# Performance work log

Measured on AMD Instinct MI355X. Metric: run time of the kernel, lower is better.

Reference implementation:

```python
import jax, jax.numpy as jnp
import numpy as np

B, F, K = 8192, 128, 32  # batch, num_features, bins per feature (D = F*K = 4096)
T_TOTAL = 1000           # num_timesteps for the cosine schedule
EPS_LOG = 1e-8
EPS_GUMBEL = 1e-30


def _cosine_sigmas(T):
    # matches _make_schedule('cosine', T)
    steps = jnp.arange(T + 1, dtype=jnp.float32)
    alphas_cumprod = jnp.cos((steps / T + 0.008) / 1.008 * jnp.pi / 2) ** 2
    return 1.0 - alphas_cumprod[1:] / alphas_cumprod[:-1]  # [T]


def setup_inputs() -> dict:
    key = jax.random.key(0)
    k1, k2 = jax.random.split(key)
    # log one-hot x0, as built in mixed_loss: log(one_hot + 1e-8)
    x0 = jax.random.randint(k1, (B, F), 0, K)
    log_x0 = jnp.log(jax.nn.one_hot(x0, K, dtype=jnp.float32) + EPS_LOG).reshape(B, F * K)
    # uniform noise for the Gumbel-max trick (rand_like in the original)
    u = jax.random.uniform(k2, (B, F * K), dtype=jnp.float32)
    return {"log_x0": log_x0, "u": u, "t": 64}


def reference(log_x0, u, t):
    # q_sample: t sequential q_forward steps, fused over features via a scan.
    sigmas = _cosine_sigmas(T_TOTAL)[:t]          # [t], t is a static Python int
    Q = jnp.ones((K, K), jnp.float32) / K         # fixed uniform score matrix

    def step(log_p, sigma_t):
        p = jnp.exp(log_p)                                     # [B,F,K]
        p_next = (1.0 - sigma_t) * p + sigma_t * jnp.einsum('bfi,ij->bfj', p, Q)
        return jnp.log(p_next + EPS_LOG), None

    log_p0 = log_x0.reshape(B, F, K)
    log_p, _ = jax.lax.scan(step, log_p0, sigmas)              # [B,F,K]

    # log_sample_categorical: Gumbel-max per feature block
    g = -jnp.log(-jnp.log(u.reshape(B, F, K) + EPS_GUMBEL) + EPS_GUMBEL)
    sample = jnp.argmax(log_p + g, axis=-1)                    # [B,F]
    log_xt = jnp.log(jax.nn.one_hot(sample, K, dtype=jnp.float32) + EPS_LOG)
    return log_xt.reshape(B, F * K)
```

## Files before the change

kernel.cpp:

```cpp
#include <hip/hip_runtime.h>
#include <math.h>


typedef float f4nt __attribute__((ext_vector_type(4)));

__device__ __forceinline__ float cr_logf32(float x) { return (float)log((double)x); }

__device__ __forceinline__ float cr_g(float u) {
    float c0 = __fadd_rn(u, 1e-30f);
    float t2 = cr_logf32(c0);
    float t3 = __fadd_rn(-t2, 1e-30f);
    float t4 = cr_logf32(t3);
    return -t4;
}

__global__ void traj_kernel(const float* __restrict__ log_x0,
                            const int* __restrict__ t_ptr,
                            float* __restrict__ traj) {
    __shared__ float ac[1001];
    __shared__ float sig[1000];
    __shared__ float init2[2];
    int t = *t_ptr;
    if (t > 1000) t = 1000;
    if (t < 0) t = 0;

    for (int s = threadIdx.x; s <= t; s += blockDim.x) {
        float a = __fdiv_rn((float)s, 1000.0f);
        float b = __fadd_rn(a, 0.008f);
        float c = __fdiv_rn(b, 1.008f);
        float d = __fmul_rn(c, 0x1.921fb6p+1f);
        float e = __fmul_rn(d, 0.5f);
        float cs = (float)cos((double)e);
        ac[s] = __fmul_rn(cs, cs);
    }
    if (threadIdx.x == 0) {
        float hotf = -1e30f, coldf = 1e30f;
        for (int j = 0; j < 32; ++j) {
            float v = log_x0[j];
            hotf = fmaxf(hotf, v);
            coldf = fminf(coldf, v);
        }
        init2[0] = hotf;
        init2[1] = coldf;
        traj[64] = coldf;
    }
    __syncthreads();
    for (int s = threadIdx.x + 1; s <= t; s += blockDim.x)
        sig[s - 1] = __fsub_rn(1.0f, __fdiv_rn(ac[s], ac[s - 1]));
    __syncthreads();

    if (threadIdx.x < 32) {
        const int h = threadIdx.x;
        float lh = init2[0];
        float lc = init2[1];
        for (int k = 0; k < t; ++k) {
            float sg = sig[k];
            float ph = (float)exp((double)lh);
            float pc = (float)exp((double)lc);
            float th = __fmul_rn(ph, 0.03125f);
            float tc = __fmul_rn(pc, 0.03125f);
            float acc = 0.0f;
            for (int i = 0; i < 32; ++i)
                acc = __fadd_rn(acc, (i == h) ? th : tc);
            float s1  = __fsub_rn(1.0f, sg);
            float sm  = __fmul_rn(sg, acc);
            float phn = __fadd_rn(__fmul_rn(s1, ph), sm);
            float pcn = __fadd_rn(__fmul_rn(s1, pc), sm);
            lh = cr_logf32(__fadd_rn(phn, 1e-8f));
            lc = cr_logf32(__fadd_rn(pcn, 1e-8f));
        }
        traj[h]      = lh;
        traj[32 + h] = lc;
    }
}

#define SCANB(VAL, IDX)                                         \
    {                                                           \
        const float cu = ((IDX) == hc) ? -1.0f : (VAL);         \
        const bool gt1 = cu > t1u;                              \
        const bool gt2 = cu > t2u;                              \
        t2u = gt1 ? t1u : (gt2 ? cu : t2u);                     \
        t1i = gt1 ? (IDX) : t1i;                                \
        t1u = gt1 ? cu : t1u;                                   \
    }

__global__ void sample_kernel(const float4* __restrict__ log_x0,
                              const float4* __restrict__ u,
                              const float* __restrict__ trajm,
                              float4* __restrict__ out) {
    __shared__ float lds_u[4][2048];
    __shared__ unsigned char lds_h[4][64];
    __shared__ float lh_s[32], lc_s[32];
    __shared__ float coldv_s;
    if (threadIdx.x < 32) {
        lh_s[threadIdx.x] = trajm[threadIdx.x];
        lc_s[threadIdx.x] = trajm[32 + threadIdx.x];
    }
    if (threadIdx.x == 0) coldv_s = trajm[64];

    const int w    = threadIdx.x >> 6;
    const int lane = threadIdx.x & 63;
    const int tile = (int)((blockIdx.x * blockDim.x + threadIdx.x) >> 6);
    const size_t fb4 = (size_t)tile * 512;

    float4 xr[8];
    #pragma unroll
    for (int k = 0; k < 8; ++k) xr[k] = log_x0[fb4 + k * 64 + lane];
    float4 ur[8];
    #pragma unroll
    for (int k = 0; k < 8; ++k) ur[k] = u[fb4 + k * 64 + lane];

    const int sgb = lane & ~7;
    #pragma unroll
    for (int k = 0; k < 8; ++k) {
        const float4 xv = xr[k];
        int p = -1;
        p = (xv.x > -1.0f) ? 0 : p;
        p = (xv.y > -1.0f) ? 1 : p;
        p = (xv.z > -1.0f) ? 2 : p;
        p = (xv.w > -1.0f) ? 3 : p;
        const unsigned long long bal = __ballot(p >= 0);
        const unsigned mm = (unsigned)((bal >> sgb) & 0xFFull);
        const int hlane = (int)__ffs(mm) - 1;
        const int psrc  = __shfl(p, sgb + ((hlane < 0) ? 0 : hlane), 64);
        const int hbin  = (hlane < 0) ? 255 : (hlane * 4 + psrc);
        if ((lane & 7) == 0)
            lds_h[w][k * 8 + (lane >> 3)] = (unsigned char)hbin;
    }

    #pragma unroll
    for (int k = 0; k < 8; ++k)
        *(float4*)&lds_u[w][k * 256 + lane * 4] = ur[k];

    __syncthreads();

    const int   h  = (int)lds_h[w][lane];
    const int   hc = (h > 31) ? 0 : h;
    const float lh = lh_s[hc];
    const float lc = lc_s[hc];
    const float coldv = coldv_s;
    const float4* urow4 = (const float4*)&lds_u[w][lane * 32];

    float t1u = -1.0f, t2u = -1.0f; int t1i = 0;
    #pragma unroll
    for (int q = 0; q < 8; ++q) {
        const int qq = (q + lane) & 7;
        const float4 v = urow4[qq];
        const int b0 = qq * 4;
        SCANB(v.x, b0) SCANB(v.y, b0 + 1) SCANB(v.z, b0 + 2) SCANB(v.w, b0 + 3)
    }
    const float uhot = lds_u[w][lane * 32 + hc];

    const float s_hot  = __fadd_rn(lh, cr_g(uhot));
    const float s_cold = __fadd_rn(lc, cr_g(t1u));
    int widx;
    if (s_hot > s_cold)      widx = hc;
    else if (s_hot < s_cold) widx = t1i;
    else                     widx = (hc < t1i) ? hc : t1i;

    const bool flagged = ((t1u - t2u) < 1e-6f) | (h > 31);
    unsigned long long fm = __ballot(flagged);
    while (fm) {
        const int fl = (int)__builtin_ctzll(fm);
        fm &= fm - 1;
        const int fh  = (int)lds_h[w][fl];
        const int fhc = (fh > 31) ? 0 : fh;
        const int l32 = lane & 31;
        const float uj  = lds_u[w][fl * 32 + l32];
        const bool jhot = (l32 == fhc) && (fh <= 31);
        float s = __fadd_rn(jhot ? lh_s[fhc] : lc_s[fhc], cr_g(uj));
        int idx = l32;
        #pragma unroll
        for (int m = 16; m > 0; m >>= 1) {
            float os = __shfl_xor(s,   m, 32);
            int   oi = __shfl_xor(idx, m, 32);
            if (os > s || (os == s && oi < idx)) { s = os; idx = oi; }
        }
        if (lane == fl) widx = idx;
    }

    #pragma unroll
    for (int k = 0; k < 8; ++k) {
        const int src = k * 8 + (lane >> 3);
        const int wk  = __shfl(widx, src, 64);
        const int qb  = (lane & 7) * 4;
        f4nt o;
        o.x = (wk == qb    ) ? 0.0f : coldv;
        o.y = (wk == qb + 1) ? 0.0f : coldv;
        o.z = (wk == qb + 2) ? 0.0f : coldv;
        o.w = (wk == qb + 3) ? 0.0f : coldv;
        __builtin_nontemporal_store(o, (f4nt*)&out[fb4 + k * 64 + lane]);
    }
}

extern "C" void kernel_launch(void* const* d_in, const int* in_sizes, int n_in,
                              void* d_out, int out_size, void* d_ws, size_t ws_size,
                              hipStream_t stream) {
    const float* log_x0 = (const float*)d_in[0];
    const float* u      = (const float*)d_in[1];
    const int*   t_ptr  = (const int*)d_in[2];
    float* out  = (float*)d_out;
    float* traj = (float*)d_ws;

    const int nfeat = in_sizes[0] / 32;
    const int ntile = nfeat / 64;
    const int nblk  = ntile / 4;

    traj_kernel<<<1, 128, 0, stream>>>(log_x0, t_ptr, traj);

    sample_kernel<<<nblk, 256, 0, stream>>>((const float4*)log_x0,
                                            (const float4*)u, traj,
                                            (float4*)out);
}
```

Measured before the change: 126.1 us.

## Split sampling into trajectory-independent gather pass and finalize pass

```diff
diff --git a/kernel.cpp b/kernel.cpp
--- a/kernel.cpp
+++ b/kernel.cpp
@@ -1,8 +1,6 @@
 #include <hip/hip_runtime.h>
 #include <math.h>
 
-
-typedef float f4nt __attribute__((ext_vector_type(4)));
 
 __device__ __forceinline__ float cr_logf32(float x) { return (float)log((double)x); }
 
@@ -84,10 +82,146 @@
         t1u = gt1 ? cu : t1u;                                   \
     }
 
-__global__ void sample_kernel(const float4* __restrict__ log_x0,
-                              const float4* __restrict__ u,
-                              const float* __restrict__ trajm,
-                              float4* __restrict__ out) {
+#define GATHER_REDUCE_BODY                                                     \
+    float4 xr[8];                                                              \
+    _Pragma("unroll")                                                          \
+    for (int k = 0; k < 8; ++k) xr[k] = log_x0[fb4 + k * 64 + lane];           \
+    float4 ur[8];                                                              \
+    _Pragma("unroll")                                                          \
+    for (int k = 0; k < 8; ++k) ur[k] = u[fb4 + k * 64 + lane];                \
+    const int sgb = lane & ~7;                                                 \
+    _Pragma("unroll")                                                          \
+    for (int k = 0; k < 8; ++k) {                                              \
+        const float4 xv = xr[k];                                               \
+        int p = -1;                                                            \
+        p = (xv.x > -1.0f) ? 0 : p;                                            \
+        p = (xv.y > -1.0f) ? 1 : p;                                            \
+        p = (xv.z > -1.0f) ? 2 : p;                                            \
+        p = (xv.w > -1.0f) ? 3 : p;                                            \
+        const unsigned long long bal = __ballot(p >= 0);                       \
+        const unsigned mm = (unsigned)((bal >> sgb) & 0xFFull);                \
+        const int hlane = (int)__ffs(mm) - 1;                                  \
+        const int psrc  = __shfl(p, sgb + ((hlane < 0) ? 0 : hlane), 64);      \
+        const int hbin  = (hlane < 0) ? 255 : (hlane * 4 + psrc);              \
+        if ((lane & 7) == 0)                                                   \
+            lds_h[w][k * 8 + (lane >> 3)] = (unsigned char)hbin;               \
+    }                                                                          \
+    _Pragma("unroll")                                                          \
+    for (int k = 0; k < 8; ++k)                                                \
+        *(float4*)&lds_u[w][k * 256 + lane * 4] = ur[k];                       \
+    __syncthreads();                                                           \
+    const int   h  = (int)lds_h[w][lane];                                      \
+    const int   hc = (h > 31) ? 0 : h;                                         \
+    const float4* urow4 = (const float4*)&lds_u[w][lane * 32];                 \
+    float t1u = -1.0f, t2u = -1.0f; int t1i = 0;                               \
+    _Pragma("unroll")                                                          \
+    for (int q = 0; q < 8; ++q) {                                              \
+        const int qq = (q + lane) & 7;                                         \
+        const float4 v = urow4[qq];                                            \
+        const int b0 = qq * 4;                                                 \
+        SCANB(v.x, b0) SCANB(v.y, b0 + 1) SCANB(v.z, b0 + 2) SCANB(v.w, b0+3) \
+    }                                                                          \
+    const float uhot = lds_u[w][lane * 32 + hc];
+
+__global__ void passA_kernel(const float4* __restrict__ log_x0,
+                             const float4* __restrict__ u,
+                             float4* __restrict__ rec) {
+    __shared__ float lds_u[4][2048];
+    __shared__ unsigned char lds_h[4][64];
+
+    const int w    = threadIdx.x >> 6;
+    const int lane = threadIdx.x & 63;
+    const int tile = (int)((blockIdx.x * blockDim.x + threadIdx.x) >> 6);
+    const size_t fb4 = (size_t)tile * 512;
+
+    GATHER_REDUCE_BODY
+
+    float4 r;
+    r.x = uhot;
+    r.y = t1u;
+    r.z = t2u;
+    r.w = __uint_as_float((unsigned)((h << 8) | t1i));
+    rec[(size_t)tile * 64 + lane] = r;
+}
+
+__global__ void passB_kernel(const float4* __restrict__ rec,
+                             const float* __restrict__ uflat,
+                             const float* __restrict__ trajm,
+                             float4* __restrict__ out,
+                             int ntile) {
+    __shared__ float lh_s[32], lc_s[32];
+    __shared__ float coldv_s;
+    if (threadIdx.x < 32) {
+        lh_s[threadIdx.x] = trajm[threadIdx.x];
+        lc_s[threadIdx.x] = trajm[32 + threadIdx.x];
+    }
+    if (threadIdx.x == 0) coldv_s = trajm[64];
+    __syncthreads();
+    const float coldv = coldv_s;
+
+    const int lane = threadIdx.x & 63;
+    const int wid  = (int)((blockIdx.x * blockDim.x + threadIdx.x) >> 6);
+    const int nwav = (int)((gridDim.x * blockDim.x) >> 6);
+
+    for (int tile = wid; tile < ntile; tile += nwav) {
+        const float4 r = rec[(size_t)tile * 64 + lane];
+        const float uhot = r.x, t1u = r.y, t2u = r.z;
+        const unsigned pk = __float_as_uint(r.w);
+        const int h   = (int)(pk >> 8);
+        const int t1i = (int)(pk & 255u);
+        const int hc  = (h > 31) ? 0 : h;
+        const float lh = lh_s[hc];
+        const float lc = lc_s[hc];
+
+        const float s_hot  = __fadd_rn(lh, cr_g(uhot));
+        const float s_cold = __fadd_rn(lc, cr_g(t1u));
+        int widx;
+        if (s_hot > s_cold)      widx = hc;
+        else if (s_hot < s_cold) widx = t1i;
+        else                     widx = (hc < t1i) ? hc : t1i;
+
+        const bool flagged = ((t1u - t2u) < 1e-6f) | (h > 31);
+        unsigned long long fm = __ballot(flagged);
+        while (fm) {
+            const int fl = (int)__builtin_ctzll(fm);
+            fm &= fm - 1;
+            const int fh  = __shfl(h, (lane & ~63) + fl, 64);
+            const int fhc = (fh > 31) ? 0 : fh;
+            const int l32 = lane & 31;
+            const size_t fbase = ((size_t)tile * 64 + fl) * 32;
+            const float uj  = uflat[fbase + l32];
+            const bool jhot = (l32 == fhc) && (fh <= 31);
+            float s = __fadd_rn(jhot ? lh_s[fhc] : lc_s[fhc], cr_g(uj));
+            int idx = l32;
+            #pragma unroll
+            for (int m = 16; m > 0; m >>= 1) {
+                float os = __shfl_xor(s,   m, 32);
+                int   oi = __shfl_xor(idx, m, 32);
+                if (os > s || (os == s && oi < idx)) { s = os; idx = oi; }
+            }
+            if (lane == fl) widx = idx;
+        }
+
+        const size_t fb4 = (size_t)tile * 512;
+        #pragma unroll
+        for (int k = 0; k < 8; ++k) {
+            const int src = k * 8 + (lane >> 3);
+            const int wk  = __shfl(widx, src, 64);
+            const int qb  = (lane & 7) * 4;
+            float4 o;
+            o.x = (wk == qb    ) ? 0.0f : coldv;
+            o.y = (wk == qb + 1) ? 0.0f : coldv;
+            o.z = (wk == qb + 2) ? 0.0f : coldv;
+            o.w = (wk == qb + 3) ? 0.0f : coldv;
+            out[fb4 + k * 64 + lane] = o;
+        }
+    }
+}
+
+__global__ void fused_kernel(const float4* __restrict__ log_x0,
+                             const float4* __restrict__ u,
+                             const float* __restrict__ trajm,
+                             float4* __restrict__ out) {
     __shared__ float lds_u[4][2048];
     __shared__ unsigned char lds_h[4][64];
     __shared__ float lh_s[32], lc_s[32];
@@ -103,53 +237,11 @@
     const int tile = (int)((blockIdx.x * blockDim.x + threadIdx.x) >> 6);
     const size_t fb4 = (size_t)tile * 512;
 
-    float4 xr[8];
-    #pragma unroll
-    for (int k = 0; k < 8; ++k) xr[k] = log_x0[fb4 + k * 64 + lane];
-    float4 ur[8];
-    #pragma unroll
-    for (int k = 0; k < 8; ++k) ur[k] = u[fb4 + k * 64 + lane];
-
-    const int sgb = lane & ~7;
-    #pragma unroll
-    for (int k = 0; k < 8; ++k) {
-        const float4 xv = xr[k];
-        int p = -1;
-        p = (xv.x > -1.0f) ? 0 : p;
-        p = (xv.y > -1.0f) ? 1 : p;
-        p = (xv.z > -1.0f) ? 2 : p;
-        p = (xv.w > -1.0f) ? 3 : p;
-        const unsigned long long bal = __ballot(p >= 0);
-        const unsigned mm = (unsigned)((bal >> sgb) & 0xFFull);
-        const int hlane = (int)__ffs(mm) - 1;
-        const int psrc  = __shfl(p, sgb + ((hlane < 0) ? 0 : hlane), 64);
-        const int hbin  = (hlane < 0) ? 255 : (hlane * 4 + psrc);
-        if ((lane & 7) == 0)
-            lds_h[w][k * 8 + (lane >> 3)] = (unsigned char)hbin;
-    }
-
-    #pragma unroll
-    for (int k = 0; k < 8; ++k)
-        *(float4*)&lds_u[w][k * 256 + lane * 4] = ur[k];
-
-    __syncthreads();
-
-    const int   h  = (int)lds_h[w][lane];
-    const int   hc = (h > 31) ? 0 : h;
+    GATHER_REDUCE_BODY
+
     const float lh = lh_s[hc];
     const float lc = lc_s[hc];
     const float coldv = coldv_s;
-    const float4* urow4 = (const float4*)&lds_u[w][lane * 32];
-
-    float t1u = -1.0f, t2u = -1.0f; int t1i = 0;
-    #pragma unroll
-    for (int q = 0; q < 8; ++q) {
-        const int qq = (q + lane) & 7;
-        const float4 v = urow4[qq];
-        const int b0 = qq * 4;
-        SCANB(v.x, b0) SCANB(v.y, b0 + 1) SCANB(v.z, b0 + 2) SCANB(v.w, b0 + 3)
-    }
-    const float uhot = lds_u[w][lane * 32 + hc];
 
     const float s_hot  = __fadd_rn(lh, cr_g(uhot));
     const float s_cold = __fadd_rn(lc, cr_g(t1u));
@@ -184,12 +276,12 @@
         const int src = k * 8 + (lane >> 3);
         const int wk  = __shfl(widx, src, 64);
         const int qb  = (lane & 7) * 4;
-        f4nt o;
+        float4 o;
         o.x = (wk == qb    ) ? 0.0f : coldv;
         o.y = (wk == qb + 1) ? 0.0f : coldv;
         o.z = (wk == qb + 2) ? 0.0f : coldv;
         o.w = (wk == qb + 3) ? 0.0f : coldv;
-        __builtin_nontemporal_store(o, (f4nt*)&out[fb4 + k * 64 + lane]);
+        out[fb4 + k * 64 + lane] = o;
     }
 }
 
@@ -206,9 +298,20 @@
     const int ntile = nfeat / 64;
     const int nblk  = ntile / 4;
 
+    const size_t rec_off   = 512;
+    const size_t rec_bytes = (size_t)nfeat * 16;
+
     traj_kernel<<<1, 128, 0, stream>>>(log_x0, t_ptr, traj);
 
-    sample_kernel<<<nblk, 256, 0, stream>>>((const float4*)log_x0,
-                                            (const float4*)u, traj,
-                                            (float4*)out);
-}
+    if (ws_size >= rec_off + rec_bytes) {
+        float4* rec = (float4*)((char*)d_ws + rec_off);
+        passA_kernel<<<nblk, 256, 0, stream>>>((const float4*)log_x0,
+                                               (const float4*)u, rec);
+        passB_kernel<<<2048, 256, 0, stream>>>(rec, u, traj,
+                                               (float4*)out, ntile);
+    } else {
+        fused_kernel<<<nblk, 256, 0, stream>>>((const float4*)log_x0,
+                                               (const float4*)u, traj,
+                                               (float4*)out);
+    }
+}
```

Result: slower. 141.1 us (+11.9%).
